# Optimization experiments

Hardware: AMD Instinct MI355X
Metric: run time of the kernel (lower is better)

## Reference

```python
import jax, jax.numpy as jnp
import numpy as np

HEADS = 16
NUM_MEM_KV = 16
SPARSE_TOPK = 8


def setup_inputs() -> dict:
    key = jax.random.key(0)
    ks = jax.random.split(key, 10)
    b, n, dim = 2, 2048, 1024
    h, dh = HEADS, 64
    inner = h * dh
    s = 0.02
    return {
        "x": jax.random.normal(ks[0], (b, n, dim), jnp.float32),
        "Wq": jax.random.normal(ks[1], (dim, inner), jnp.float32) * s,
        "Wk": jax.random.normal(ks[2], (dim, inner), jnp.float32) * s,
        "Wv": jax.random.normal(ks[3], (dim, inner), jnp.float32) * s,
        "pre_proj": jax.random.normal(ks[4], (h, h), jnp.float32),
        "post_proj": jax.random.normal(ks[5], (h, h), jnp.float32),
        "mem_k": jax.random.normal(ks[6], (h, NUM_MEM_KV, dh), jnp.float32),
        "mem_v": jax.random.normal(ks[7], (h, NUM_MEM_KV, dh), jnp.float32),
        "Wo": jax.random.normal(ks[8], (inner, dim), jnp.float32) * s,
        "bo": jnp.zeros((dim,), jnp.float32),
    }


def reference(x, Wq, Wk, Wv, pre_proj, post_proj, mem_k, mem_v, Wo, bo):
    b, n, dim = x.shape
    h = HEADS
    dh = Wq.shape[1] // h
    nm = mem_k.shape[1]
    scale = dh ** -0.5

    def split_heads(t):  # [b, n, h*dh] -> [b, h, n, dh]
        return t.reshape(b, -1, h, dh).transpose(0, 2, 1, 3)

    q = split_heads(x @ Wq)
    k = split_heads(x @ Wk)
    v = split_heads(x @ Wv)

    # prepend learned memory key/values: j = nm + n
    k = jnp.concatenate([jnp.broadcast_to(mem_k[None], (b, h, nm, dh)), k], axis=2)
    v = jnp.concatenate([jnp.broadcast_to(mem_v[None], (b, h, nm, dh)), v], axis=2)

    dots = jnp.einsum("bhid,bhjd->bhij", q, k) * scale  # [b, h, n, nm+n]
    mask_value = -jnp.finfo(dots.dtype).max

    # talking heads (pre-softmax): mix across the head dimension
    dots = jnp.einsum("bhij,hk->bkij", dots, pre_proj)

    # causal mask, shifted by nm mem slots (mem positions always visible)
    j = nm + n
    causal = jnp.arange(n)[:, None] < (jnp.arange(j)[None, :] - nm)  # True = masked
    dots = jnp.where(causal[None, None], mask_value, dots)

    # sparse top-k pruning along the key axis
    top = jax.lax.top_k(dots, SPARSE_TOPK)[0]
    thresh = top[..., -1:]
    dots = jnp.where(dots < thresh, mask_value, dots)

    attn = jax.nn.softmax(dots, axis=-1)

    # talking heads (post-softmax)
    attn = jnp.einsum("bhij,hk->bkij", attn, post_proj)

    out = jnp.einsum("bhij,bhjd->bhid", attn, v)
    out = out.transpose(0, 2, 1, 3).reshape(b, n, h * dh)
    return out @ Wo + bo
```

## Files before the change

### kernel.cpp

```cpp
#include <hip/hip_runtime.h>
#include <hip/hip_bf16.h>

typedef unsigned short u16;
typedef unsigned int   u32;

#define BB   2
#define NN   2048
#define HS   16
#define DH   64
#define NM   16
#define JT   2064
#define DIM  1024
#define JC   5
#define NBB  256
#define TOTT 8384

#define SPLITSZ ((size_t)BB * HS * JT * DH)

__device__ __forceinline__ float bfval(u16 u) { return __uint_as_float(((u32)u) << 16); }
__device__ __forceinline__ float lo16(u32 u)  { return __uint_as_float(u << 16); }
__device__ __forceinline__ float hi16(u32 u)  { return __uint_as_float(u & 0xffff0000u); }
__device__ __forceinline__ u16 f2bf(float f)
{
    __hip_bfloat16 h = __float2bfloat16(f);
    return *(u16*)&h;
}

__device__ __forceinline__ int blk_start(int k) { return (131 * k) >> 2; }
__device__ __forceinline__ int blk_of(int g)
{
    int k = (4 * g) / 131;
    while (blk_start(k + 1) <= g) ++k;
    while (blk_start(k) > g) --k;
    return k;
}
__device__ __forceinline__ int row_start(int iy) { return (iy * (iy + 3)) >> 1; }

typedef __bf16 bf16x8 __attribute__((ext_vector_type(8)));
typedef float  f32x4  __attribute__((ext_vector_type(4)));

#define MFMA16(A, B, C) __builtin_amdgcn_mfma_f32_16x16x32_bf16(A, B, C, 0, 0, 0)

__global__ void prep_mem_kernel(const float* __restrict__ mem_k, u16* __restrict__ k_sp)
{
    int t = blockIdx.x * 256 + threadIdx.x;
    int d = t & 63, j = (t >> 6) & 15, h = (t >> 10) & 15, b = (t >> 14) & 1;
    float x = mem_k[(h * NM + j) * DH + d];
    size_t di = ((size_t)(b * HS + h) * JT + j) * DH + d;
    u16 sh = f2bf(x);
    float d1 = x - bfval(sh);
    u16 sm = f2bf(d1);
    u16 sl = f2bf(d1 - bfval(sm));
    k_sp[di] = sh; k_sp[di + SPLITSZ] = sm; k_sp[di + 2 * SPLITSZ] = sl;
}

__global__ void prep_wot_kernel(const float* __restrict__ Wo, u16* __restrict__ wot)
{
    int t = blockIdx.x * 256 + threadIdx.x;
    int k = t & 1023, n = t >> 10;
    wot[(size_t)n * 1024 + k] = f2bf(Wo[(size_t)k * 1024 + n]);
}

__global__ __launch_bounds__(256) void gemm_kernel(
    const float* __restrict__ A, const float* __restrict__ Bw,
    u16* __restrict__ dst16, float* __restrict__ dstf, int mode)
{
    __shared__ __align__(16) u16 a_h[128][32];
    __shared__ __align__(16) u16 a_m[128][32];
    __shared__ __align__(16) u16 a_l[128][32];
    __shared__ __align__(16) u16 b_hT[64][32];
    __shared__ __align__(16) u16 b_mT[64][32];
    __shared__ __align__(16) u16 b_lT[64][32];

    const int tid  = threadIdx.x;
    const int m0   = blockIdx.x * 128;
    const int n0   = blockIdx.y * 64;
    const int wave = tid >> 6, lane = tid & 63;
    const int ln16 = lane & 15, quad = lane >> 4;

    const int arow = tid >> 1;
    const int ac   = (tid & 1) * 16;
    const int brow = tid >> 3;
    const int bc   = (tid & 7) * 8;

    f32x4 acc[8] = {};

    for (int k0 = 0; k0 < 1024; k0 += 32) {
        float av[16];
        {
            const float4* ap = (const float4*)&A[(size_t)(m0 + arow) * 1024 + k0 + ac];
            *(float4*)&av[0]  = ap[0]; *(float4*)&av[4]  = ap[1];
            *(float4*)&av[8]  = ap[2]; *(float4*)&av[12] = ap[3];
        }
        float bv[8];
        {
            const float4* bp = (const float4*)&Bw[(size_t)(k0 + brow) * 1024 + n0 + bc];
            *(float4*)&bv[0] = bp[0]; *(float4*)&bv[4] = bp[1];
        }
        u16 ah[16], am[16], al[16], bh[8], bm[8], bl[8];
        #pragma unroll
        for (int e = 0; e < 16; ++e) {
            ah[e] = f2bf(av[e]);
            float d1 = av[e] - bfval(ah[e]);
            am[e] = f2bf(d1);
            al[e] = (mode != 0) ? f2bf(d1 - bfval(am[e])) : (u16)0;
        }
        #pragma unroll
        for (int e = 0; e < 8; ++e) {
            bh[e] = f2bf(bv[e]);
            float d1 = bv[e] - bfval(bh[e]);
            bm[e] = f2bf(d1);
            bl[e] = (mode != 0) ? f2bf(d1 - bfval(bm[e])) : (u16)0;
        }
        __syncthreads();
        *(uint4*)&a_h[arow][ac]     = ((uint4*)ah)[0];
        *(uint4*)&a_h[arow][ac + 8] = ((uint4*)ah)[1];
        *(uint4*)&a_m[arow][ac]     = ((uint4*)am)[0];
        *(uint4*)&a_m[arow][ac + 8] = ((uint4*)am)[1];
        if (mode != 0) {
            *(uint4*)&a_l[arow][ac]     = ((uint4*)al)[0];
            *(uint4*)&a_l[arow][ac + 8] = ((uint4*)al)[1];
        }
        #pragma unroll
        for (int e = 0; e < 8; ++e) {
            b_hT[bc + e][brow] = bh[e];
            b_mT[bc + e][brow] = bm[e];
            if (mode != 0) b_lT[bc + e][brow] = bl[e];
        }
        __syncthreads();

        bf16x8 a0h = *(const bf16x8*)&a_h[wave * 32 + ln16][quad * 8];
        bf16x8 a0m = *(const bf16x8*)&a_m[wave * 32 + ln16][quad * 8];
        bf16x8 a1h = *(const bf16x8*)&a_h[wave * 32 + 16 + ln16][quad * 8];
        bf16x8 a1m = *(const bf16x8*)&a_m[wave * 32 + 16 + ln16][quad * 8];
        bf16x8 a0l = {}, a1l = {};
        if (mode != 0) {
            a0l = *(const bf16x8*)&a_l[wave * 32 + ln16][quad * 8];
            a1l = *(const bf16x8*)&a_l[wave * 32 + 16 + ln16][quad * 8];
        }
        #pragma unroll
        for (int c = 0; c < 4; ++c) {
            bf16x8 bh_ = *(const bf16x8*)&b_hT[c * 16 + ln16][quad * 8];
            bf16x8 bm_ = *(const bf16x8*)&b_mT[c * 16 + ln16][quad * 8];
            acc[c]     = MFMA16(a0m, bm_, acc[c]);
            acc[c]     = MFMA16(a0h, bm_, acc[c]);
            acc[c]     = MFMA16(a0m, bh_, acc[c]);
            acc[c]     = MFMA16(a0h, bh_, acc[c]);
            acc[4 + c] = MFMA16(a1m, bm_, acc[4 + c]);
            acc[4 + c] = MFMA16(a1h, bm_, acc[4 + c]);
            acc[4 + c] = MFMA16(a1m, bh_, acc[4 + c]);
            acc[4 + c] = MFMA16(a1h, bh_, acc[4 + c]);
            if (mode != 0) {
                bf16x8 bl_ = *(const bf16x8*)&b_lT[c * 16 + ln16][quad * 8];
                acc[c]     = MFMA16(a0h, bl_, acc[c]);
                acc[c]     = MFMA16(a0l, bh_, acc[c]);
                acc[4 + c] = MFMA16(a1h, bl_, acc[4 + c]);
                acc[4 + c] = MFMA16(a1l, bh_, acc[4 + c]);
            }
        }
    }

    #pragma unroll
    for (int hf = 0; hf < 2; ++hf) {
        #pragma unroll
        for (int c = 0; c < 4; ++c) {
            #pragma unroll
            for (int r = 0; r < 4; ++r) {
                int row = m0 + wave * 32 + hf * 16 + quad * 4 + r;
                int col = n0 + c * 16 + ln16;
                float v = acc[hf * 4 + c][r];
                if (mode == 1) {
                    dstf[(size_t)row * 1024 + col] = v;
                } else {
                    int b = row >> 11, i = row & 2047;
                    int hd = col >> 6, d = col & 63;
                    if (mode == 0) {
                        dst16[(((size_t)(b * HS + hd)) * NN + i) * DH + d] = f2bf(v);
                    } else {
                        size_t di = (((size_t)(b * HS + hd)) * JT + NM + i) * DH + d;
                        u16 sh = f2bf(v);
                        float d1 = v - bfval(sh);
                        u16 sm = f2bf(d1);
                        u16 sl = f2bf(d1 - bfval(sm));
                        dst16[di] = sh;
                        dst16[di + SPLITSZ] = sm;
                        dst16[di + 2 * SPLITSZ] = sl;
                    }
                }
            }
        }
    }
}

__global__ __launch_bounds__(512) void score_topk_kernel(
    const u16* __restrict__ k_hi, const u16* __restrict__ k_mi,
    const u16* __restrict__ k_lo,
    const float* __restrict__ q_all, const float* __restrict__ pre,
    float* __restrict__ ws_val, u16* __restrict__ ws_idx)
{
    const int bid = blockIdx.x;
    const int b   = bid >> 8;
    const int kb  = bid & 255;

    int g = blk_start(kb);
    const int gend = blk_start(kb + 1);

    __shared__ __align__(16) float fsm[12544];
    float* S   = fsm;
    float* pp  = fsm + 8192;
    float* scr = fsm + 8448;

    const int tid  = threadIdx.x;
    const int wave = tid >> 6, lane = tid & 63;
    const int ln16 = lane & 15, quad = lane >> 4;

    if (tid < 256) pp[tid] = pre[tid] * 0.125f;
    __syncthreads();

    const int kk_r = (wave & 3) * 4 + (lane & 3);
    const int ti_r = lane >> 2;
    const int tjh  = wave >> 2;
    const int srow = kk_r * 16 + ti_r;

    const u32 kbase0 = ((u32)(b * HS) * JT + (u32)ln16) * DH + (u32)(quad * 8);
    const u32 hstep  = (u32)(JT * DH);
    const u32 kbA    = kbase0 + (u32)(wave * 2) * hstep;
    const u32 kbB    = kbA + hstep;

    int iy = (int)((sqrtf((float)(8 * g + 9)) - 3.0f) * 0.5f);
    while (row_start(iy + 1) <= g) ++iy;
    while (row_start(iy) > g) --iy;

    bf16x8 pA0h, pA0m, pA0l, pA1h, pA1m, pA1l;
    bf16x8 pB0h, pB0m, pB0l, pB1h, pB1m, pB1l;
    {
        const u32 j0 = (u32)((g - row_start(iy)) * 16) * DH;
        pA0h = *(const bf16x8*)(k_hi + kbA + j0);
        pA0m = *(const bf16x8*)(k_mi + kbA + j0);
        pA0l = *(const bf16x8*)(k_lo + kbA + j0);
        pA1h = *(const bf16x8*)(k_hi + kbA + j0 + 32u);
        pA1m = *(const bf16x8*)(k_mi + kbA + j0 + 32u);
        pA1l = *(const bf16x8*)(k_lo + kbA + j0 + 32u);
        pB0h = *(const bf16x8*)(k_hi + kbB + j0);
        pB0m = *(const bf16x8*)(k_mi + kbB + j0);
        pB0l = *(const bf16x8*)(k_lo + kbB + j0);
        pB1h = *(const bf16x8*)(k_hi + kbB + j0 + 32u);
        pB1m = *(const bf16x8*)(k_mi + kbB + j0 + 32u);
        pB1l = *(const bf16x8*)(k_lo + kbB + j0 + 32u);
    }

    while (g < gend) {
        const int ntiles = iy + 2;
        const int Srow0  = row_start(iy);
        int jt = g - Srow0;
        const int nrow   = min(ntiles - jt, gend - g);
        const int jt_hi  = jt + nrow;
        const int i0     = iy * 16;
        const int slot   = kb - blk_of(Srow0);

        bf16x8 qh[2][2], qm[2][2], ql[2][2];
        {
            const float* qrow = q_all + (size_t)(b * NN + i0 + ln16) * DIM;
            #pragma unroll
            for (int h2 = 0; h2 < 2; ++h2) {
                const int h = wave * 2 + h2;
                #pragma unroll
                for (int half = 0; half < 2; ++half) {
                    const float* src = qrow + h * 64 + half * 32 + quad * 8;
                    float4 u0 = *(const float4*)src;
                    float4 u1 = *(const float4*)(src + 4);
                    float xv[8] = {u0.x, u0.y, u0.z, u0.w, u1.x, u1.y, u1.z, u1.w};
                    u16 eh[8], em[8], el[8];
                    #pragma unroll
                    for (int e = 0; e < 8; ++e) {
                        eh[e] = f2bf(xv[e]);
                        float d1 = xv[e] - bfval(eh[e]);
                        em[e] = f2bf(d1);
                        el[e] = f2bf(d1 - bfval(em[e]));
                    }
                    qh[h2][half] = *(bf16x8*)eh;
                    qm[h2][half] = *(bf16x8*)em;
                    ql[h2][half] = *(bf16x8*)el;
                }
            }
        }

        float tv[8];
        int   tx[8];
        #pragma unroll
        for (int t = 0; t < 8; ++t) { tv[t] = -1e30f; tx[t] = 0; }
        const int jlim = NM + i0 + ti_r;

        int par = 0;
        for (; jt < jt_hi; ++jt, par ^= 1) {
            float* Sb = S + par * 4096;

            {
                f32x4 acc = {};
                acc = MFMA16(qm[0][0], pA0m, acc);
                acc = MFMA16(qh[0][0], pA0l, acc);
                acc = MFMA16(ql[0][0], pA0h, acc);
                acc = MFMA16(qh[0][0], pA0m, acc);
                acc = MFMA16(qm[0][0], pA0h, acc);
                acc = MFMA16(qh[0][0], pA0h, acc);
                acc = MFMA16(qm[0][1], pA1m, acc);
                acc = MFMA16(qh[0][1], pA1l, acc);
                acc = MFMA16(ql[0][1], pA1h, acc);
                acc = MFMA16(qh[0][1], pA1m, acc);
                acc = MFMA16(qm[0][1], pA1h, acc);
                acc = MFMA16(qh[0][1], pA1h, acc);
                const int h = wave * 2;
                #pragma unroll
                for (int r = 0; r < 4; ++r) {
                    int i   = quad * 4 + r;
                    int rot = ((ln16 >> 2) + i + (i >> 2)) & 3;
                    Sb[h * 256 + i * 16 + rot * 4 + (ln16 & 3)] = acc[r];
                }
            }
            {
                f32x4 acc = {};
                acc = MFMA16(qm[1][0], pB0m, acc);
                acc = MFMA16(qh[1][0], pB0l, acc);
                acc = MFMA16(ql[1][0], pB0h, acc);
                acc = MFMA16(qh[1][0], pB0m, acc);
                acc = MFMA16(qm[1][0], pB0h, acc);
                acc = MFMA16(qh[1][0], pB0h, acc);
                acc = MFMA16(qm[1][1], pB1m, acc);
                acc = MFMA16(qh[1][1], pB1l, acc);
                acc = MFMA16(ql[1][1], pB1h, acc);
                acc = MFMA16(qh[1][1], pB1m, acc);
                acc = MFMA16(qm[1][1], pB1h, acc);
                acc = MFMA16(qh[1][1], pB1h, acc);
                const int h = wave * 2 + 1;
                #pragma unroll
                for (int r = 0; r < 4; ++r) {
                    int i   = quad * 4 + r;
                    int rot = ((ln16 >> 2) + i + (i >> 2)) & 3;
                    Sb[h * 256 + i * 16 + rot * 4 + (ln16 & 3)] = acc[r];
                }
            }

            {
                const int jt_next = (jt + 1 < jt_hi) ? jt + 1 : 0;
                const u32 jn = (u32)(jt_next * 16) * DH;
                pA0h = *(const bf16x8*)(k_hi + kbA + jn);
                pA0m = *(const bf16x8*)(k_mi + kbA + jn);
                pA0l = *(const bf16x8*)(k_lo + kbA + jn);
                pA1h = *(const bf16x8*)(k_hi + kbA + jn + 32u);
                pA1m = *(const bf16x8*)(k_mi + kbA + jn + 32u);
                pA1l = *(const bf16x8*)(k_lo + kbA + jn + 32u);
                pB0h = *(const bf16x8*)(k_hi + kbB + jn);
                pB0m = *(const bf16x8*)(k_mi + kbB + jn);
                pB0l = *(const bf16x8*)(k_lo + kbB + jn);
                pB1h = *(const bf16x8*)(k_hi + kbB + jn + 32u);
                pB1m = *(const bf16x8*)(k_mi + kbB + jn + 32u);
                pB1l = *(const bf16x8*)(k_lo + kbB + jn + 32u);
            }

            asm volatile("s_waitcnt lgkmcnt(0)" ::: "memory");
            __builtin_amdgcn_s_barrier();
            __builtin_amdgcn_sched_barrier(0);

            const int jb = jt * 16;
            #pragma unroll
            for (int tc = 0; tc < 2; ++tc) {
                const int tjc = tjh * 2 + tc;
                const int rot = (tjc + ti_r + (ti_r >> 2)) & 3;
                const float* sp = Sb + ti_r * 16 + rot * 4;
                f32x4 m = {};
                #pragma unroll
                for (int h = 0; h < 16; ++h) {
                    float w  = pp[h * 16 + kk_r];
                    f32x4 s4 = *(const f32x4*)(sp + h * 256);
                    m += s4 * w;
                }
                const int jb2 = jb + tjc * 4;
                #pragma unroll
                for (int e = 0; e < 4; ++e) {
                    float c = m[e];
                    int j = jb2 + e;
                    if (j <= jlim && c > tv[7]) {
                        #pragma unroll
                        for (int t = 7; t >= 1; --t) {
                            if (c > tv[t - 1])      { tv[t] = tv[t - 1]; tx[t] = tx[t - 1]; }
                            else if (c > tv[t])     { tv[t] = c;         tx[t] = j; }
                        }
                        if (c > tv[0]) { tv[0] = c; tx[0] = j; }
                    }
                }
            }
        }

        __syncthreads();
        if (tjh == 1) {
            #pragma unroll
            for (int t = 0; t < 8; ++t) {
                scr[srow * 8 + t]        = tv[t];
                scr[2048 + srow * 8 + t] = __int_as_float(tx[t]);
            }
        }
        __syncthreads();
        if (tjh == 0) {
            #pragma unroll
            for (int t2 = 0; t2 < 8; ++t2) {
                float c = scr[srow * 8 + t2];
                int   j = __float_as_int(scr[2048 + srow * 8 + t2]);
                if (c > tv[7]) {
                    #pragma unroll
                    for (int t = 7; t >= 1; --t) {
                        if (c > tv[t - 1])      { tv[t] = tv[t - 1]; tx[t] = tx[t - 1]; }
                        else if (c > tv[t])     { tv[t] = c;         tx[t] = j; }
                    }
                    if (c > tv[0]) { tv[0] = c; tx[0] = j; }
                }
            }
            size_t base = ((((size_t)b * HS + kk_r) * NN + i0 + ti_r) * JC + slot) * 8;
            #pragma unroll
            for (int t = 0; t < 8; ++t) {
                ws_val[base + t] = tv[t];
                ws_idx[base + t] = (u16)tx[t];
            }
        }

        g += nrow;
        ++iy;
    }
}

__global__ __launch_bounds__(512) void merge_pv_kernel(
    const u16* __restrict__ v_bf, const float* __restrict__ mem_v,
    const float* __restrict__ ws_val, const u16* __restrict__ ws_idx,
    const float* __restrict__ post, const u16* __restrict__ wot,
    const float* __restrict__ bo, float* __restrict__ out)
{
    __shared__ __align__(16) float fsm[13312];
    float* dotsm = fsm + 8704;
    float* pp2   = fsm + 13056;
    u16*   arows = (u16*)fsm;

    const int tid = threadIdx.x;
    const int b   = blockIdx.y;
    const int i0  = blockIdx.x * 16;
    const int ntiles = blockIdx.x + 2;
    const int Srow0  = row_start(blockIdx.x);
    const int jc_cnt = blk_of(Srow0 + ntiles - 1) - blk_of(Srow0) + 1;

    if (tid < 256) pp2[tid] = post[tid];

    if (tid < 256) {
        const int kk_r = tid & 15, ti_r = tid >> 4;

        float tv[8];
        int   tx[8];
        #pragma unroll
        for (int t = 0; t < 8; ++t) { tv[t] = -1e30f; tx[t] = 0; }

        size_t rbase = (((size_t)b * HS + kk_r) * NN + i0 + ti_r) * JC;
        for (int jc = 0; jc < jc_cnt; ++jc) {
            #pragma unroll
            for (int t2 = 0; t2 < 8; ++t2) {
                float c = ws_val[(rbase + jc) * 8 + t2];
                int   j = ws_idx[(rbase + jc) * 8 + t2];
                if (c > tv[7]) {
                    #pragma unroll
                    for (int t = 7; t >= 1; --t) {
                        if (c > tv[t - 1])      { tv[t] = tv[t - 1]; tx[t] = tx[t - 1]; }
                        else if (c > tv[t])     { tv[t] = c;         tx[t] = j; }
                    }
                    if (c > tv[0]) { tv[0] = c; tx[0] = j; }
                }
            }
        }

        float m = tv[0];
        float wv[8], wsum = 0.f;
        #pragma unroll
        for (int t = 0; t < 8; ++t) { wv[t] = __expf(tv[t] - m); wsum += wv[t]; }
        float inv = 1.f / wsum;

        #pragma unroll
        for (int t = 0; t < 8; ++t) {
            dotsm[(kk_r * 16 + ti_r) * 8 + t]        = wv[t] * inv;
            dotsm[2048 + (kk_r * 16 + ti_r) * 8 + t] = __int_as_float(tx[t]);
        }
    }
    __syncthreads();

    {
        const int ti_o = (tid & 255) >> 4, k2 = tid & 15, dh = tid >> 8;
        float acc[32];
        #pragma unroll
        for (int d = 0; d < 32; ++d) acc[d] = 0.f;
        const u16*   vws_base  = v_bf + (size_t)(b * HS + k2) * NN * DH + dh * 32;
        const float* vmem_base = mem_v + (size_t)k2 * NM * DH + dh * 32;

        for (int kk = 0; kk < 16; ++kk) {
            float p2 = pp2[kk * 16 + k2];
            for (int t = 0; t < 8; ++t) {
                float w = dotsm[(kk * 16 + ti_o) * 8 + t] * p2;
                int j = __float_as_int(dotsm[2048 + (kk * 16 + ti_o) * 8 + t]);
                if (j < NM) {
                    const float* vr = vmem_base + (size_t)j * DH;
                    #pragma unroll
                    for (int r = 0; r < 8; ++r) {
                        float4 u = *(const float4*)&vr[r * 4];
                        acc[r * 4 + 0] += w * u.x; acc[r * 4 + 1] += w * u.y;
                        acc[r * 4 + 2] += w * u.z; acc[r * 4 + 3] += w * u.w;
                    }
                } else {
                    const uint4* vr = (const uint4*)(vws_base + (size_t)(j - NM) * DH);
                    #pragma unroll
                    for (int r = 0; r < 4; ++r) {
                        uint4 u = vr[r];
                        acc[r * 8 + 0] += w * lo16(u.x); acc[r * 8 + 1] += w * hi16(u.x);
                        acc[r * 8 + 2] += w * lo16(u.y); acc[r * 8 + 3] += w * hi16(u.y);
                        acc[r * 8 + 4] += w * lo16(u.z); acc[r * 8 + 5] += w * hi16(u.z);
                        acc[r * 8 + 6] += w * lo16(u.w); acc[r * 8 + 7] += w * hi16(u.w);
                    }
                }
            }
        }
        #pragma unroll
        for (int d = 0; d < 32; ++d) {
            float o = acc[d];
            o = (o == o) ? o : 1e4f;
            arows[ti_o * 1032 + k2 * 64 + dh * 32 + d] = f2bf(o);
        }
    }
    __syncthreads();

    const int wave = tid >> 6, lane = tid & 63;
    const int ln16 = lane & 15, quad = lane >> 4;

    f32x4 oacc[8];
    #pragma unroll
    for (int t = 0; t < 8; ++t) {
        float bv = bo[(t * 8 + wave) * 16 + ln16];
        oacc[t][0] = bv; oacc[t][1] = bv; oacc[t][2] = bv; oacc[t][3] = bv;
    }

    for (int k0 = 0; k0 < 1024; k0 += 32) {
        bf16x8 af = *(const bf16x8*)&arows[ln16 * 1032 + k0 + quad * 8];
        #pragma unroll
        for (int t = 0; t < 8; ++t) {
            const int n = (t * 8 + wave) * 16 + ln16;
            bf16x8 bf_ = *(const bf16x8*)&wot[(size_t)n * 1024 + k0 + quad * 8];
            oacc[t] = MFMA16(af, bf_, oacc[t]);
        }
    }

    #pragma unroll
    for (int t = 0; t < 8; ++t) {
        const int n = (t * 8 + wave) * 16 + ln16;
        #pragma unroll
        for (int r = 0; r < 4; ++r) {
            int row = quad * 4 + r;
            out[(size_t)(b * NN + i0 + row) * DIM + n] = oacc[t][r];
        }
    }
}

extern "C" void kernel_launch(void* const* d_in, const int* in_sizes, int n_in,
                              void* d_out, int out_size, void* d_ws, size_t ws_size,
                              hipStream_t stream)
{
    (void)in_sizes; (void)n_in; (void)out_size; (void)ws_size;
    const float* x     = (const float*)d_in[0];
    const float* Wq    = (const float*)d_in[1];
    const float* Wk    = (const float*)d_in[2];
    const float* Wv    = (const float*)d_in[3];
    const float* pre   = (const float*)d_in[4];
    const float* post  = (const float*)d_in[5];
    const float* mem_k = (const float*)d_in[6];
    const float* mem_v = (const float*)d_in[7];
    const float* Wo    = (const float*)d_in[8];
    const float* bo    = (const float*)d_in[9];

    u16*   k_sp   = (u16*)d_ws;
    u16*   v_bf   = k_sp + 3 * SPLITSZ;
    float* ws_val = (float*)(v_bf + (size_t)BB * HS * NN * DH);
    u16*   ws_idx = (u16*)(ws_val + (size_t)BB * HS * NN * JC * 8);
    u16*   wot    = ws_idx + (size_t)BB * HS * NN * JC * 8;
    float* q_tmp  = (float*)d_out;

    prep_mem_kernel<<<128, 256, 0, stream>>>(mem_k, k_sp);
    prep_wot_kernel<<<4096, 256, 0, stream>>>(Wo, wot);

    dim3 gg(32, 16);
    gemm_kernel<<<gg, 256, 0, stream>>>(x, Wq, nullptr, q_tmp, 1);
    gemm_kernel<<<gg, 256, 0, stream>>>(x, Wk, k_sp, nullptr, 2);
    gemm_kernel<<<gg, 256, 0, stream>>>(x, Wv, v_bf, nullptr, 0);

    score_topk_kernel<<<512, 512, 0, stream>>>(k_sp, k_sp + SPLITSZ,
                                               k_sp + 2 * SPLITSZ,
                                               (const float*)d_out,
                                               pre, ws_val, ws_idx);

    dim3 ga(128, 2);
    merge_pv_kernel<<<ga, 512, 0, stream>>>(v_bf, mem_v, ws_val, ws_idx,
                                            post, wot, bo, (float*)d_out);
}
```

Before: 972.8 us.

## Prefetch next GEMM K-tile into registers and tile the Wo transpose via LDS

The projection GEMM now issues the global loads for the next K-slice right after writing the current slice to LDS, so load latency overlaps the MFMA work. The full __syncthreads calls are replaced by explicit lgkmcnt waits plus s_barrier, which leaves outstanding global loads pending across the barrier. The Wo transpose kernel switches from strided per-element transposition to a 32x32 shared-memory tiled transpose with coalesced reads and writes. The prefetch adds register pressure and one redundant wrap-around load on the last iteration.

```diff
diff --git a/kernel.cpp b/kernel.cpp
--- a/kernel.cpp
+++ b/kernel.cpp
@@ -54,11 +54,21 @@
     k_sp[di] = sh; k_sp[di + SPLITSZ] = sm; k_sp[di + 2 * SPLITSZ] = sl;
 }
 
-__global__ void prep_wot_kernel(const float* __restrict__ Wo, u16* __restrict__ wot)
-{
-    int t = blockIdx.x * 256 + threadIdx.x;
-    int k = t & 1023, n = t >> 10;
-    wot[(size_t)n * 1024 + k] = f2bf(Wo[(size_t)k * 1024 + n]);
+__global__ __launch_bounds__(256) void prep_wot_kernel(
+    const float* __restrict__ Wo, u16* __restrict__ wot)
+{
+    __shared__ u16 t[32][33];
+    const int bx = blockIdx.x & 31;
+    const int by = blockIdx.x >> 5;
+    const int tx = threadIdx.x & 31, ty = threadIdx.x >> 5;
+
+    #pragma unroll
+    for (int i = 0; i < 32; i += 8)
+        t[ty + i][tx] = f2bf(Wo[(size_t)(by * 32 + ty + i) * 1024 + bx * 32 + tx]);
+    __syncthreads();
+    #pragma unroll
+    for (int i = 0; i < 32; i += 8)
+        wot[(size_t)(bx * 32 + ty + i) * 1024 + by * 32 + tx] = t[tx][ty + i];
 }
 
 __global__ __launch_bounds__(256) void gemm_kernel(
@@ -83,20 +93,21 @@
     const int brow = tid >> 3;
     const int bc   = (tid & 7) * 8;
 
+    const float* aptr = &A[(size_t)(m0 + arow) * 1024 + ac];
+    const float* bptr = &Bw[(size_t)brow * 1024 + n0 + bc];
+
     f32x4 acc[8] = {};
 
+    float av[16], bv[8];
+    {
+        const float4* ap = (const float4*)aptr;
+        *(float4*)&av[0]  = ap[0]; *(float4*)&av[4]  = ap[1];
+        *(float4*)&av[8]  = ap[2]; *(float4*)&av[12] = ap[3];
+        const float4* bp = (const float4*)bptr;
+        *(float4*)&bv[0] = bp[0]; *(float4*)&bv[4] = bp[1];
+    }
+
     for (int k0 = 0; k0 < 1024; k0 += 32) {
-        float av[16];
-        {
-            const float4* ap = (const float4*)&A[(size_t)(m0 + arow) * 1024 + k0 + ac];
-            *(float4*)&av[0]  = ap[0]; *(float4*)&av[4]  = ap[1];
-            *(float4*)&av[8]  = ap[2]; *(float4*)&av[12] = ap[3];
-        }
-        float bv[8];
-        {
-            const float4* bp = (const float4*)&Bw[(size_t)(k0 + brow) * 1024 + n0 + bc];
-            *(float4*)&bv[0] = bp[0]; *(float4*)&bv[4] = bp[1];
-        }
         u16 ah[16], am[16], al[16], bh[8], bm[8], bl[8];
         #pragma unroll
         for (int e = 0; e < 16; ++e) {
@@ -112,7 +123,10 @@
             bm[e] = f2bf(d1);
             bl[e] = (mode != 0) ? f2bf(d1 - bfval(bm[e])) : (u16)0;
         }
-        __syncthreads();
+
+        asm volatile("s_waitcnt lgkmcnt(0)" ::: "memory");
+        __builtin_amdgcn_s_barrier();
+
         *(uint4*)&a_h[arow][ac]     = ((uint4*)ah)[0];
         *(uint4*)&a_h[arow][ac + 8] = ((uint4*)ah)[1];
         *(uint4*)&a_m[arow][ac]     = ((uint4*)am)[0];
@@ -127,7 +141,19 @@
             b_mT[bc + e][brow] = bm[e];
             if (mode != 0) b_lT[bc + e][brow] = bl[e];
         }
-        __syncthreads();
+
+        {
+            const int kn = (k0 + 32 < 1024) ? k0 + 32 : 0;
+            const float4* ap = (const float4*)(aptr + kn);
+            *(float4*)&av[0]  = ap[0]; *(float4*)&av[4]  = ap[1];
+            *(float4*)&av[8]  = ap[2]; *(float4*)&av[12] = ap[3];
+            const float4* bp = (const float4*)(bptr + (size_t)kn * 1024);
+            *(float4*)&bv[0] = bp[0]; *(float4*)&bv[4] = bp[1];
+        }
+
+        asm volatile("s_waitcnt lgkmcnt(0)" ::: "memory");
+        __builtin_amdgcn_s_barrier();
+        __builtin_amdgcn_sched_barrier(0);
 
         bf16x8 a0h = *(const bf16x8*)&a_h[wave * 32 + ln16][quad * 8];
         bf16x8 a0m = *(const bf16x8*)&a_m[wave * 32 + ln16][quad * 8];
@@ -584,7 +610,7 @@
     float* q_tmp  = (float*)d_out;
 
     prep_mem_kernel<<<128, 256, 0, stream>>>(mem_k, k_sp);
-    prep_wot_kernel<<<4096, 256, 0, stream>>>(Wo, wot);
+    prep_wot_kernel<<<1024, 256, 0, stream>>>(Wo, wot);
 
     dim3 gg(32, 16);
     gemm_kernel<<<gg, 256, 0, stream>>>(x, Wq, nullptr, q_tmp, 1);
```

Result: no change. 962.3 us (-1.1%).
